# Kernel tuning notes

Hardware: AMD Instinct MI355X
Metric: run time of the kernel (lower is better)

## Reference

```python
import jax, jax.numpy as jnp
import numpy as np

N_NODES = 50000
N_EDGES = 800000
NUM_GRAPHS = 512


def gcn_conv(x, edge_index, W, b, num_nodes):
    # PyG GCNConv: h = D^{-1/2} (A + I) D^{-1/2} (x @ W) + b
    h = x @ W
    src, dst = edge_index[0], edge_index[1]
    loop = jnp.arange(num_nodes)
    src = jnp.concatenate([src, loop])
    dst = jnp.concatenate([dst, loop])
    deg = jax.ops.segment_sum(jnp.ones_like(dst, dtype=h.dtype), dst,
                              num_segments=num_nodes)
    dinv = jnp.where(deg > 0, jax.lax.rsqrt(deg), 0.0)
    norm = dinv[src] * dinv[dst]                      # [E+N]
    msg = h[src] * norm[:, None]                      # gather + scale
    out = jax.ops.segment_sum(msg, dst, num_segments=num_nodes)  # scatter-add
    return out + b


def global_mean_pool(x, batch, num_graphs):
    sums = jax.ops.segment_sum(x, batch, num_segments=num_graphs)
    cnts = jax.ops.segment_sum(jnp.ones((x.shape[0],), x.dtype), batch,
                               num_segments=num_graphs)
    return sums / jnp.maximum(cnts, 1.0)[:, None]


def setup_inputs() -> dict:
    key = jax.random.key(0)
    ks = jax.random.split(key, 8)
    x = jax.random.normal(ks[0], (N_NODES, 128), dtype=jnp.float32)
    edge_index = jax.random.randint(ks[1], (2, N_EDGES), 0, N_NODES, dtype=jnp.int64)
    batch = jnp.sort(jax.random.randint(ks[2], (N_NODES,), 0, NUM_GRAPHS, dtype=jnp.int64))
    W1 = jax.random.normal(ks[3], (128, 128), dtype=jnp.float32) * (1.0 / np.sqrt(128))
    b1 = jnp.zeros((128,), jnp.float32)
    W2 = jax.random.normal(ks[4], (128, 64), dtype=jnp.float32) * (1.0 / np.sqrt(128))
    b2 = jnp.zeros((64,), jnp.float32)
    Wl = jax.random.normal(ks[5], (64, 64), dtype=jnp.float32) * (1.0 / np.sqrt(64))
    bl = jnp.zeros((64,), jnp.float32)
    return {"x": x, "edge_index": edge_index, "batch": batch,
            "W1": W1, "b1": b1, "W2": W2, "b2": b2, "Wl": Wl, "bl": bl}


def reference(x, edge_index, batch, W1, b1, W2, b2, Wl, bl):
    num_nodes = x.shape[0]
    h = gcn_conv(x, edge_index, W1, b1, num_nodes)
    h = jax.nn.relu(h)
    h = gcn_conv(h, edge_index, W2, b2, num_nodes)
    g = global_mean_pool(h, batch, NUM_GRAPHS)
    # dropout p=0.5 is identity in eval mode
    return g @ Wl + bl
```

## Files before the change

kernel.cpp:

```cpp
#include <hip/hip_runtime.h>
#include <hip/hip_fp16.h>
#include <math.h>


#define FEAT1 128
#define FEAT2 64
#define BCAP 8192

using half8 = __attribute__((ext_vector_type(8))) _Float16;
using f32x4 = __attribute__((ext_vector_type(4))) float;

__global__ __launch_bounds__(256) void prep(const float* __restrict__ W1,
                                            const float* __restrict__ W2,
                                            _Float16* __restrict__ Wt1,
                                            _Float16* __restrict__ Wt2,
                                            int* __restrict__ bcur,
                                            float* __restrict__ pooled,
                                            int nb, int npool) {
    const int i = blockIdx.x * 256 + threadIdx.x;
    if (i < nb) bcur[i] = 0;
    const int j = i - nb;
    if (j >= 0 && j < npool) pooled[j] = 0.0f;
    if (i < 128 * 128) {
        int k = i & 127, c = i >> 7;
        Wt1[c * 128 + k] = (_Float16)W1[k * 128 + c];
    }
    if (i < 64 * 128) {
        int k = i & 127, c = i >> 7;
        Wt2[c * 128 + k] = (_Float16)W2[k * 64 + c];
    }
}


__global__ __launch_bounds__(256) void bin_scatter(const int* __restrict__ esrc,
                                                   const int* __restrict__ edst,
                                                   int ne, int nb,
                                                   int* __restrict__ bucket_cursor,
                                                   int* __restrict__ ebin) {
    __shared__ int lcnt[256];
    __shared__ int lcur[256];
    const int tid = threadIdx.x;
    const int e0 = blockIdx.x * 8192;
    int dcache[32];
    lcnt[tid] = 0;
    __syncthreads();
    #pragma unroll
    for (int k = 0; k < 32; k++) {
        int e = e0 + k * 256 + tid;
        dcache[k] = (e < ne) ? edst[e] : -1;
        if (dcache[k] >= 0) atomicAdd(&lcnt[dcache[k] >> 8], 1);
    }
    __syncthreads();
    if (tid < nb && lcnt[tid] > 0)
        lcur[tid] = atomicAdd(&bucket_cursor[tid], lcnt[tid]);
    __syncthreads();
    #pragma unroll
    for (int k = 0; k < 32; k++) {
        int d = dcache[k];
        if (d >= 0) {
            int e = e0 + k * 256 + tid;
            int b = d >> 8;
            int p = atomicAdd(&lcur[b], 1);
            if (p < BCAP)
                ebin[b * BCAP + p] = esrc[e] | ((d & 255) << 18);
        }
    }
}

__global__ __launch_bounds__(256) void bucket_csr(const int* __restrict__ ebin,
                                                  const int* __restrict__ bucket_cursor,
                                                  int n_nodes,
                                                  int* __restrict__ csr,
                                                  int2* __restrict__ nodeinfo,
                                                  float* __restrict__ dinv) {
    __shared__ int lcnt[256];
    __shared__ int lscan[256];
    __shared__ int lcur[256];
    const int b = blockIdx.x;
    const int tid = threadIdx.x;
    const int ebeg = b * BCAP;
    int cnt_b = bucket_cursor[b];
    if (cnt_b > BCAP) cnt_b = BCAP;
    const int eend = ebeg + cnt_b;
    lcnt[tid] = 0;
    __syncthreads();
    for (int e = ebeg + tid; e < eend; e += 256)
        atomicAdd(&lcnt[(ebin[e] >> 18) & 255], 1);
    __syncthreads();
    int v = lcnt[tid];
    lscan[tid] = v;
    __syncthreads();
    for (int off = 1; off < 256; off <<= 1) {
        int u = (tid >= off) ? lscan[tid - off] : 0;
        __syncthreads();
        lscan[tid] += u;
        __syncthreads();
    }
    const int start = ebeg + (lscan[tid] - v);
    const int node = (b << 8) + tid;
    if (node < n_nodes) {
        nodeinfo[node] = make_int2(start, v);
        dinv[node] = (float)(1.0 / sqrt((double)(v + 1)));
    }
    lcur[tid] = start;
    __syncthreads();
    for (int e = ebeg + tid; e < eend; e += 256) {
        int pk = ebin[e];
        int p = atomicAdd(&lcur[(pk >> 18) & 255], 1);
        csr[p] = pk & 0x3FFFF;
    }
}

template <int FOUT, bool A_F16>
__global__ __launch_bounds__(256) void gemm_direct(const void* __restrict__ Aptr,
                                                   const _Float16* __restrict__ Wt,
                                                   const float* __restrict__ dinv,
                                                   _Float16* __restrict__ out, int n) {
    const int wv = threadIdx.x >> 6;
    const int lane = threadIdx.x & 63;
    const int row0 = blockIdx.x * 128 + wv * 32;
    const int r16 = lane & 15;
    const int kb = (lane >> 4) * 8;

    half8 afrag[2][4];
    #pragma unroll
    for (int mi = 0; mi < 2; mi++) {
        const int grow = row0 + mi * 16 + r16;
        #pragma unroll
        for (int ks = 0; ks < 4; ks++) {
            if constexpr (A_F16) {
                half8 v = {};
                if (grow < n)
                    v = *(const half8*)((const _Float16*)Aptr + (size_t)grow * 128 + ks * 32 + kb);
                afrag[mi][ks] = v;
            } else {
                float4 v0 = {0.f, 0.f, 0.f, 0.f}, v1 = {0.f, 0.f, 0.f, 0.f};
                if (grow < n) {
                    const float* p = (const float*)Aptr + (size_t)grow * 128 + ks * 32 + kb;
                    v0 = *(const float4*)(p);
                    v1 = *(const float4*)(p + 4);
                }
                afrag[mi][ks] = half8{(_Float16)v0.x, (_Float16)v0.y, (_Float16)v0.z, (_Float16)v0.w,
                                      (_Float16)v1.x, (_Float16)v1.y, (_Float16)v1.z, (_Float16)v1.w};
            }
        }
    }

    #pragma unroll
    for (int ct = 0; ct < FOUT / 64; ct++) {
        const int col0 = ct * 64;
        f32x4 acc[2][4] = {};
        #pragma unroll
        for (int ks = 0; ks < 4; ks++) {
            #pragma unroll
            for (int nj = 0; nj < 4; nj++) {
                half8 b = *(const half8*)(Wt + (size_t)(col0 + nj * 16 + r16) * 128 + ks * 32 + kb);
                acc[0][nj] = __builtin_amdgcn_mfma_f32_16x16x32_f16(afrag[0][ks], b, acc[0][nj], 0, 0, 0);
                acc[1][nj] = __builtin_amdgcn_mfma_f32_16x16x32_f16(afrag[1][ks], b, acc[1][nj], 0, 0, 0);
            }
        }
        #pragma unroll
        for (int mi = 0; mi < 2; mi++) {
            const int gr0 = row0 + mi * 16 + (lane >> 4) * 4;
            #pragma unroll
            for (int r = 0; r < 4; r++) {
                const int grow = gr0 + r;
                if (grow < n) {
                    const float s = dinv[grow];
                    #pragma unroll
                    for (int nj = 0; nj < 4; nj++) {
                        out[(size_t)grow * FOUT + col0 + nj * 16 + r16] =
                            (_Float16)(acc[mi][nj][r] * s);
                    }
                }
            }
        }
    }
}

__global__ __launch_bounds__(256) void aggregate_l1(const __half* __restrict__ t,
                                                    const float* __restrict__ dinv,
                                                    const int2* __restrict__ nodeinfo,
                                                    const int* __restrict__ csr_src,
                                                    const float* __restrict__ bias,
                                                    __half* __restrict__ outp, int n) {
    constexpr int F = 128;
    const int wv = threadIdx.x >> 6;
    const int lane = threadIdx.x & 63;
    const int i = blockIdx.x * 4 + wv;
    if (i >= n) return;
    const float di = dinv[i];
    const int2 ni = nodeinfo[i];
    const int e0 = ni.x, e1 = ni.x + ni.y;

    float2 a0, a1 = {0.f, 0.f}, a2 = {0.f, 0.f}, a3 = {0.f, 0.f};
    a0 = __half22float2(((const __half2*)(t + (size_t)i * F))[lane]);
    int e = e0;
    for (; e + 8 <= e1; e += 8) {
        int s0 = csr_src[e + 0], s1 = csr_src[e + 1], s2 = csr_src[e + 2], s3 = csr_src[e + 3];
        int s4 = csr_src[e + 4], s5 = csr_src[e + 5], s6 = csr_src[e + 6], s7 = csr_src[e + 7];
        float2 v0 = __half22float2(((const __half2*)(t + (size_t)s0 * F))[lane]);
        float2 v1 = __half22float2(((const __half2*)(t + (size_t)s1 * F))[lane]);
        float2 v2 = __half22float2(((const __half2*)(t + (size_t)s2 * F))[lane]);
        float2 v3 = __half22float2(((const __half2*)(t + (size_t)s3 * F))[lane]);
        float2 v4 = __half22float2(((const __half2*)(t + (size_t)s4 * F))[lane]);
        float2 v5 = __half22float2(((const __half2*)(t + (size_t)s5 * F))[lane]);
        float2 v6 = __half22float2(((const __half2*)(t + (size_t)s6 * F))[lane]);
        float2 v7 = __half22float2(((const __half2*)(t + (size_t)s7 * F))[lane]);
        a0.x += v0.x + v4.x; a0.y += v0.y + v4.y;
        a1.x += v1.x + v5.x; a1.y += v1.y + v5.y;
        a2.x += v2.x + v6.x; a2.y += v2.y + v6.y;
        a3.x += v3.x + v7.x; a3.y += v3.y + v7.y;
    }
    for (; e + 4 <= e1; e += 4) {
        int s0 = csr_src[e + 0], s1 = csr_src[e + 1], s2 = csr_src[e + 2], s3 = csr_src[e + 3];
        float2 v0 = __half22float2(((const __half2*)(t + (size_t)s0 * F))[lane]);
        float2 v1 = __half22float2(((const __half2*)(t + (size_t)s1 * F))[lane]);
        float2 v2 = __half22float2(((const __half2*)(t + (size_t)s2 * F))[lane]);
        float2 v3 = __half22float2(((const __half2*)(t + (size_t)s3 * F))[lane]);
        a0.x += v0.x; a0.y += v0.y;
        a1.x += v1.x; a1.y += v1.y;
        a2.x += v2.x; a2.y += v2.y;
        a3.x += v3.x; a3.y += v3.y;
    }
    for (; e < e1; e++) {
        int s = csr_src[e];
        float2 v = __half22float2(((const __half2*)(t + (size_t)s * F))[lane]);
        a0.x += v.x; a0.y += v.y;
    }
    float2 b = ((const float2*)bias)[lane];
    float rx = (a0.x + a1.x + a2.x + a3.x) * di + b.x;
    float ry = (a0.y + a1.y + a2.y + a3.y) * di + b.y;
    rx = fmaxf(rx, 0.f); ry = fmaxf(ry, 0.f);
    ((__half2*)(outp + (size_t)i * F))[lane] = __floats2half2_rn(rx, ry);
}

__global__ __launch_bounds__(256) void aggregate_pool(const __half* __restrict__ t,
                                                      const float* __restrict__ dinv,
                                                      const int2* __restrict__ nodeinfo,
                                                      const int* __restrict__ csr_src,
                                                      const int* __restrict__ batch,
                                                      float* __restrict__ pooled_sums, int n) {
    constexpr int F = 64;
    const int wv = threadIdx.x >> 6;
    const int lane = threadIdx.x & 63;
    const int i = blockIdx.x * 4 + wv;
    if (i >= n) return;
    const float di = dinv[i];
    const int2 ni = nodeinfo[i];
    const int e0 = ni.x, e1 = ni.x + ni.y;

    float a0, a1 = 0.f, a2 = 0.f, a3 = 0.f;
    a0 = __half2float(t[(size_t)i * F + lane]);
    int e = e0;
    for (; e + 8 <= e1; e += 8) {
        int s0 = csr_src[e + 0], s1 = csr_src[e + 1], s2 = csr_src[e + 2], s3 = csr_src[e + 3];
        int s4 = csr_src[e + 4], s5 = csr_src[e + 5], s6 = csr_src[e + 6], s7 = csr_src[e + 7];
        float v0 = __half2float(t[(size_t)s0 * F + lane]);
        float v1 = __half2float(t[(size_t)s1 * F + lane]);
        float v2 = __half2float(t[(size_t)s2 * F + lane]);
        float v3 = __half2float(t[(size_t)s3 * F + lane]);
        float v4 = __half2float(t[(size_t)s4 * F + lane]);
        float v5 = __half2float(t[(size_t)s5 * F + lane]);
        float v6 = __half2float(t[(size_t)s6 * F + lane]);
        float v7 = __half2float(t[(size_t)s7 * F + lane]);
        a0 += v0 + v4; a1 += v1 + v5; a2 += v2 + v6; a3 += v3 + v7;
    }
    for (; e + 4 <= e1; e += 4) {
        int s0 = csr_src[e + 0], s1 = csr_src[e + 1], s2 = csr_src[e + 2], s3 = csr_src[e + 3];
        a0 += __half2float(t[(size_t)s0 * F + lane]);
        a1 += __half2float(t[(size_t)s1 * F + lane]);
        a2 += __half2float(t[(size_t)s2 * F + lane]);
        a3 += __half2float(t[(size_t)s3 * F + lane]);
    }
    for (; e < e1; e++) {
        a0 += __half2float(t[(size_t)csr_src[e] * F + lane]);
    }
    float r = (a0 + a1 + a2 + a3) * di;
    const int g = batch[i];
    atomicAdd(&pooled_sums[(size_t)g * F + lane], r);
}

__global__ __launch_bounds__(64) void classify(const float* __restrict__ pooled_sums,
                                               const int* __restrict__ batch, int n,
                                               const float* __restrict__ b2,
                                               const float* __restrict__ Wl,
                                               const float* __restrict__ bl,
                                               float* __restrict__ out) {
    __shared__ float pr[64];
    const int g = blockIdx.x;
    const int lane = threadIdx.x;
    int lo = 0, hi = n;
    while (lo < hi) { int mid = (lo + hi) >> 1; if (batch[mid] < g) lo = mid + 1; else hi = mid; }
    const int start = lo;
    hi = n;
    while (lo < hi) { int mid = (lo + hi) >> 1; if (batch[mid] < g + 1) lo = mid + 1; else hi = mid; }
    const float cnt = (float)(lo - start);
    float p = pooled_sums[(size_t)g * 64 + lane] / fmaxf(cnt, 1.0f) + b2[lane];
    pr[lane] = p;
    __syncthreads();
    float acc = bl[lane];
    #pragma unroll 8
    for (int k = 0; k < 64; k++) acc += pr[k] * Wl[k * 64 + lane];
    out[(size_t)g * 64 + lane] = acc;
}


extern "C" void kernel_launch(void* const* d_in, const int* in_sizes, int n_in,
                              void* d_out, int out_size, void* d_ws, size_t ws_size,
                              hipStream_t stream) {
    const float* x    = (const float*)d_in[0];
    const int*   eidx = (const int*)d_in[1];
    const int*   batch= (const int*)d_in[2];
    const float* W1   = (const float*)d_in[3];
    const float* b1   = (const float*)d_in[4];
    const float* W2   = (const float*)d_in[5];
    const float* b2   = (const float*)d_in[6];
    const float* Wl   = (const float*)d_in[7];
    const float* bl   = (const float*)d_in[8];
    float* out = (float*)d_out;

    const int n_nodes  = in_sizes[0] / FEAT1;
    const int n_edges  = in_sizes[1] / 2;
    const int n_graphs = out_size / FEAT2;
    const int* esrc = eidx;
    const int* edst = eidx + n_edges;
    const int nb = (n_nodes + 255) >> 8;
    const int npool = n_graphs * FEAT2;

    char* ws = (char*)d_ws;
    size_t off = 0;
    auto alloc = [&](size_t bytes) -> void* {
        void* p = ws + off;
        off += (bytes + 255) & ~(size_t)255;
        return p;
    };
    _Float16* t1     = (_Float16*)alloc((size_t)n_nodes * FEAT1 * 2);
    __half*   h1h    = (__half*)alloc((size_t)n_nodes * FEAT1 * 2);
    float*    dinv   = (float*)alloc((size_t)n_nodes * 4);
    int2*   nodeinfo = (int2*)alloc((size_t)n_nodes * 8);
    int*    bcur     = (int*)alloc((size_t)nb * 4);
    float*  pooled   = (float*)alloc((size_t)npool * 4);
    _Float16* Wt1    = (_Float16*)alloc(128 * 128 * 2);
    _Float16* Wt2    = (_Float16*)alloc(64 * 128 * 2);
    int*    ebin     = (int*)alloc((size_t)nb * BCAP * 4);
    int*    csr      = (int*)alloc((size_t)nb * BCAP * 4);

    const int nrb = (n_nodes + 127) / 128;

    prep<<<(nb + npool + 255) / 256, 256, 0, stream>>>(W1, W2, Wt1, Wt2, bcur, pooled, nb, npool);
    bin_scatter<<<(n_edges + 8191) / 8192, 256, 0, stream>>>(esrc, edst, n_edges, nb, bcur, ebin);
    bucket_csr<<<nb, 256, 0, stream>>>(ebin, bcur, n_nodes, csr, nodeinfo, dinv);

    gemm_direct<FEAT1, false><<<nrb, 256, 0, stream>>>(x, Wt1, dinv, t1, n_nodes);
    aggregate_l1<<<(n_nodes + 3) / 4, 256, 0, stream>>>(
        (const __half*)t1, dinv, nodeinfo, csr, b1, h1h, n_nodes);

    gemm_direct<FEAT2, true><<<nrb, 256, 0, stream>>>(h1h, Wt2, dinv, t1, n_nodes);
    aggregate_pool<<<(n_nodes + 3) / 4, 256, 0, stream>>>(
        (const __half*)t1, dinv, nodeinfo, csr, batch, pooled, n_nodes);

    classify<<<n_graphs, 64, 0, stream>>>(pooled, batch, n_nodes, b2, Wl, bl, out);
}
```

Before: 151.4 us.

## Fuse CSR build with layer-1 GEMM and layer-1 aggregation with layer-2 GEMM

The bucket CSR build and the layer-1 GEMM now run as one launch, with different block ranges doing independent work. The GEMM no longer needs the degree scaling, which moves into the gather as a per-source dinv multiply. The layer-1 aggregation now does the layer-2 GEMM per node through an LDS staging buffer and MFMA, so the intermediate h1 buffer is never written to or read from global memory. bin_scatter uses smaller per-block edge chunks. The costs are extra dinv gathers per edge and MFMA work wasted on replicated single-row tiles.

Result: slower. 197.5 us (+30.4%).

```diff
diff --git a/kernel.cpp b/kernel.cpp
--- a/kernel.cpp
+++ b/kernel.cpp
@@ -31,7 +31,6 @@
     }
 }
 
-
 __global__ __launch_bounds__(256) void bin_scatter(const int* __restrict__ esrc,
                                                    const int* __restrict__ edst,
                                                    int ne, int nb,
@@ -40,12 +39,12 @@
     __shared__ int lcnt[256];
     __shared__ int lcur[256];
     const int tid = threadIdx.x;
-    const int e0 = blockIdx.x * 8192;
-    int dcache[32];
+    const int e0 = blockIdx.x * 2048;
+    int dcache[8];
     lcnt[tid] = 0;
     __syncthreads();
     #pragma unroll
-    for (int k = 0; k < 32; k++) {
+    for (int k = 0; k < 8; k++) {
         int e = e0 + k * 256 + tid;
         dcache[k] = (e < ne) ? edst[e] : -1;
         if (dcache[k] >= 0) atomicAdd(&lcnt[dcache[k] >> 8], 1);
@@ -55,7 +54,7 @@
         lcur[tid] = atomicAdd(&bucket_cursor[tid], lcnt[tid]);
     __syncthreads();
     #pragma unroll
-    for (int k = 0; k < 32; k++) {
+    for (int k = 0; k < 8; k++) {
         int d = dcache[k];
         if (d >= 0) {
             int e = e0 + k * 256 + tid;
@@ -67,76 +66,68 @@
     }
 }
 
-__global__ __launch_bounds__(256) void bucket_csr(const int* __restrict__ ebin,
-                                                  const int* __restrict__ bucket_cursor,
-                                                  int n_nodes,
-                                                  int* __restrict__ csr,
-                                                  int2* __restrict__ nodeinfo,
-                                                  float* __restrict__ dinv) {
-    __shared__ int lcnt[256];
-    __shared__ int lscan[256];
-    __shared__ int lcur[256];
-    const int b = blockIdx.x;
-    const int tid = threadIdx.x;
-    const int ebeg = b * BCAP;
-    int cnt_b = bucket_cursor[b];
-    if (cnt_b > BCAP) cnt_b = BCAP;
-    const int eend = ebeg + cnt_b;
-    lcnt[tid] = 0;
-    __syncthreads();
-    for (int e = ebeg + tid; e < eend; e += 256)
-        atomicAdd(&lcnt[(ebin[e] >> 18) & 255], 1);
-    __syncthreads();
-    int v = lcnt[tid];
-    lscan[tid] = v;
-    __syncthreads();
-    for (int off = 1; off < 256; off <<= 1) {
-        int u = (tid >= off) ? lscan[tid - off] : 0;
+__global__ __launch_bounds__(256) void csr_gemm1(const int* __restrict__ ebin,
+                                                 const int* __restrict__ bucket_cursor,
+                                                 int n_nodes, int nb,
+                                                 int* __restrict__ csr,
+                                                 int2* __restrict__ nodeinfo,
+                                                 float* __restrict__ dinv,
+                                                 const float* __restrict__ A,
+                                                 const _Float16* __restrict__ Wt1,
+                                                 _Float16* __restrict__ t1raw) {
+    if ((int)blockIdx.x < nb) {
+        __shared__ int lcnt[256];
+        __shared__ int lscan[256];
+        __shared__ int lcur[256];
+        const int b = blockIdx.x;
+        const int tid = threadIdx.x;
+        const int ebeg = b * BCAP;
+        int cnt_b = bucket_cursor[b];
+        if (cnt_b > BCAP) cnt_b = BCAP;
+        const int eend = ebeg + cnt_b;
+        lcnt[tid] = 0;
         __syncthreads();
-        lscan[tid] += u;
+        for (int e = ebeg + tid; e < eend; e += 256)
+            atomicAdd(&lcnt[(ebin[e] >> 18) & 255], 1);
         __syncthreads();
-    }
-    const int start = ebeg + (lscan[tid] - v);
-    const int node = (b << 8) + tid;
-    if (node < n_nodes) {
-        nodeinfo[node] = make_int2(start, v);
-        dinv[node] = (float)(1.0 / sqrt((double)(v + 1)));
-    }
-    lcur[tid] = start;
-    __syncthreads();
-    for (int e = ebeg + tid; e < eend; e += 256) {
-        int pk = ebin[e];
-        int p = atomicAdd(&lcur[(pk >> 18) & 255], 1);
-        csr[p] = pk & 0x3FFFF;
-    }
-}
-
-template <int FOUT, bool A_F16>
-__global__ __launch_bounds__(256) void gemm_direct(const void* __restrict__ Aptr,
-                                                   const _Float16* __restrict__ Wt,
-                                                   const float* __restrict__ dinv,
-                                                   _Float16* __restrict__ out, int n) {
-    const int wv = threadIdx.x >> 6;
-    const int lane = threadIdx.x & 63;
-    const int row0 = blockIdx.x * 128 + wv * 32;
-    const int r16 = lane & 15;
-    const int kb = (lane >> 4) * 8;
-
-    half8 afrag[2][4];
-    #pragma unroll
-    for (int mi = 0; mi < 2; mi++) {
-        const int grow = row0 + mi * 16 + r16;
+        int v = lcnt[tid];
+        lscan[tid] = v;
+        __syncthreads();
+        for (int off = 1; off < 256; off <<= 1) {
+            int u = (tid >= off) ? lscan[tid - off] : 0;
+            __syncthreads();
+            lscan[tid] += u;
+            __syncthreads();
+        }
+        const int start = ebeg + (lscan[tid] - v);
+        const int node = (b << 8) + tid;
+        if (node < n_nodes) {
+            nodeinfo[node] = make_int2(start, v);
+            dinv[node] = (float)(1.0 / sqrt((double)(v + 1)));
+        }
+        lcur[tid] = start;
+        __syncthreads();
+        for (int e = ebeg + tid; e < eend; e += 256) {
+            int pk = ebin[e];
+            int p = atomicAdd(&lcur[(pk >> 18) & 255], 1);
+            csr[p] = pk & 0x3FFFF;
+        }
+    } else {
+        const int wv = threadIdx.x >> 6;
+        const int lane = threadIdx.x & 63;
+        const int row0 = (blockIdx.x - nb) * 128 + wv * 32;
+        const int r16 = lane & 15;
+        const int kb = (lane >> 4) * 8;
+
+        half8 afrag[2][4];
         #pragma unroll
-        for (int ks = 0; ks < 4; ks++) {
-            if constexpr (A_F16) {
-                half8 v = {};
-                if (grow < n)
-                    v = *(const half8*)((const _Float16*)Aptr + (size_t)grow * 128 + ks * 32 + kb);
-                afrag[mi][ks] = v;
-            } else {
+        for (int mi = 0; mi < 2; mi++) {
+            const int grow = row0 + mi * 16 + r16;
+            #pragma unroll
+            for (int ks = 0; ks < 4; ks++) {
                 float4 v0 = {0.f, 0.f, 0.f, 0.f}, v1 = {0.f, 0.f, 0.f, 0.f};
-                if (grow < n) {
-                    const float* p = (const float*)Aptr + (size_t)grow * 128 + ks * 32 + kb;
+                if (grow < n_nodes) {
+                    const float* p = A + (size_t)grow * 128 + ks * 32 + kb;
                     v0 = *(const float4*)(p);
                     v1 = *(const float4*)(p + 4);
                 }
@@ -144,33 +135,30 @@
                                       (_Float16)v1.x, (_Float16)v1.y, (_Float16)v1.z, (_Float16)v1.w};
             }
         }
-    }
-
-    #pragma unroll
-    for (int ct = 0; ct < FOUT / 64; ct++) {
-        const int col0 = ct * 64;
-        f32x4 acc[2][4] = {};
         #pragma unroll
-        for (int ks = 0; ks < 4; ks++) {
+        for (int ct = 0; ct < 2; ct++) {
+            const int col0 = ct * 64;
+            f32x4 acc[2][4] = {};
             #pragma unroll
-            for (int nj = 0; nj < 4; nj++) {
-                half8 b = *(const half8*)(Wt + (size_t)(col0 + nj * 16 + r16) * 128 + ks * 32 + kb);
-                acc[0][nj] = __builtin_amdgcn_mfma_f32_16x16x32_f16(afrag[0][ks], b, acc[0][nj], 0, 0, 0);
-                acc[1][nj] = __builtin_amdgcn_mfma_f32_16x16x32_f16(afrag[1][ks], b, acc[1][nj], 0, 0, 0);
+            for (int ks = 0; ks < 4; ks++) {
+                #pragma unroll
+                for (int nj = 0; nj < 4; nj++) {
+                    half8 b = *(const half8*)(Wt1 + (size_t)(col0 + nj * 16 + r16) * 128 + ks * 32 + kb);
+                    acc[0][nj] = __builtin_amdgcn_mfma_f32_16x16x32_f16(afrag[0][ks], b, acc[0][nj], 0, 0, 0);
+                    acc[1][nj] = __builtin_amdgcn_mfma_f32_16x16x32_f16(afrag[1][ks], b, acc[1][nj], 0, 0, 0);
+                }
             }
-        }
-        #pragma unroll
-        for (int mi = 0; mi < 2; mi++) {
-            const int gr0 = row0 + mi * 16 + (lane >> 4) * 4;
             #pragma unroll
-            for (int r = 0; r < 4; r++) {
-                const int grow = gr0 + r;
-                if (grow < n) {
-                    const float s = dinv[grow];
-                    #pragma unroll
-                    for (int nj = 0; nj < 4; nj++) {
-                        out[(size_t)grow * FOUT + col0 + nj * 16 + r16] =
-                            (_Float16)(acc[mi][nj][r] * s);
+            for (int mi = 0; mi < 2; mi++) {
+                const int gr0 = row0 + mi * 16 + (lane >> 4) * 4;
+                #pragma unroll
+                for (int r = 0; r < 4; r++) {
+                    const int grow = gr0 + r;
+                    if (grow < n_nodes) {
+                        #pragma unroll
+                        for (int nj = 0; nj < 4; nj++)
+                            t1raw[(size_t)grow * 128 + col0 + nj * 16 + r16] =
+                                (_Float16)acc[mi][nj][r];
                     }
                 }
             }
@@ -178,13 +166,15 @@
     }
 }
 
-__global__ __launch_bounds__(256) void aggregate_l1(const __half* __restrict__ t,
-                                                    const float* __restrict__ dinv,
-                                                    const int2* __restrict__ nodeinfo,
-                                                    const int* __restrict__ csr_src,
-                                                    const float* __restrict__ bias,
-                                                    __half* __restrict__ outp, int n) {
+__global__ __launch_bounds__(256) void agg1_gemm2(const __half* __restrict__ t,
+                                                  const float* __restrict__ dinv,
+                                                  const int2* __restrict__ nodeinfo,
+                                                  const int* __restrict__ csr_src,
+                                                  const float* __restrict__ bias,
+                                                  const _Float16* __restrict__ Wt2,
+                                                  _Float16* __restrict__ t2, int n) {
     constexpr int F = 128;
+    __shared__ _Float16 hlds[4][128];
     const int wv = threadIdx.x >> 6;
     const int lane = threadIdx.x & 63;
     const int i = blockIdx.x * 4 + wv;
@@ -194,11 +184,16 @@
     const int e0 = ni.x, e1 = ni.x + ni.y;
 
     float2 a0, a1 = {0.f, 0.f}, a2 = {0.f, 0.f}, a3 = {0.f, 0.f};
-    a0 = __half22float2(((const __half2*)(t + (size_t)i * F))[lane]);
+    {
+        float2 v = __half22float2(((const __half2*)(t + (size_t)i * F))[lane]);
+        a0.x = v.x * di; a0.y = v.y * di;
+    }
     int e = e0;
     for (; e + 8 <= e1; e += 8) {
         int s0 = csr_src[e + 0], s1 = csr_src[e + 1], s2 = csr_src[e + 2], s3 = csr_src[e + 3];
         int s4 = csr_src[e + 4], s5 = csr_src[e + 5], s6 = csr_src[e + 6], s7 = csr_src[e + 7];
+        float d0 = dinv[s0], d1 = dinv[s1], d2 = dinv[s2], d3 = dinv[s3];
+        float d4 = dinv[s4], d5 = dinv[s5], d6 = dinv[s6], d7 = dinv[s7];
         float2 v0 = __half22float2(((const __half2*)(t + (size_t)s0 * F))[lane]);
         float2 v1 = __half22float2(((const __half2*)(t + (size_t)s1 * F))[lane]);
         float2 v2 = __half22float2(((const __half2*)(t + (size_t)s2 * F))[lane]);
@@ -207,32 +202,52 @@
         float2 v5 = __half22float2(((const __half2*)(t + (size_t)s5 * F))[lane]);
         float2 v6 = __half22float2(((const __half2*)(t + (size_t)s6 * F))[lane]);
         float2 v7 = __half22float2(((const __half2*)(t + (size_t)s7 * F))[lane]);
-        a0.x += v0.x + v4.x; a0.y += v0.y + v4.y;
-        a1.x += v1.x + v5.x; a1.y += v1.y + v5.y;
-        a2.x += v2.x + v6.x; a2.y += v2.y + v6.y;
-        a3.x += v3.x + v7.x; a3.y += v3.y + v7.y;
+        a0.x += v0.x * d0 + v4.x * d4; a0.y += v0.y * d0 + v4.y * d4;
+        a1.x += v1.x * d1 + v5.x * d5; a1.y += v1.y * d1 + v5.y * d5;
+        a2.x += v2.x * d2 + v6.x * d6; a2.y += v2.y * d2 + v6.y * d6;
+        a3.x += v3.x * d3 + v7.x * d7; a3.y += v3.y * d3 + v7.y * d7;
     }
     for (; e + 4 <= e1; e += 4) {
         int s0 = csr_src[e + 0], s1 = csr_src[e + 1], s2 = csr_src[e + 2], s3 = csr_src[e + 3];
+        float d0 = dinv[s0], d1 = dinv[s1], d2 = dinv[s2], d3 = dinv[s3];
         float2 v0 = __half22float2(((const __half2*)(t + (size_t)s0 * F))[lane]);
         float2 v1 = __half22float2(((const __half2*)(t + (size_t)s1 * F))[lane]);
         float2 v2 = __half22float2(((const __half2*)(t + (size_t)s2 * F))[lane]);
         float2 v3 = __half22float2(((const __half2*)(t + (size_t)s3 * F))[lane]);
-        a0.x += v0.x; a0.y += v0.y;
-        a1.x += v1.x; a1.y += v1.y;
-        a2.x += v2.x; a2.y += v2.y;
-        a3.x += v3.x; a3.y += v3.y;
+        a0.x += v0.x * d0; a0.y += v0.y * d0;
+        a1.x += v1.x * d1; a1.y += v1.y * d1;
+        a2.x += v2.x * d2; a2.y += v2.y * d2;
+        a3.x += v3.x * d3; a3.y += v3.y * d3;
     }
     for (; e < e1; e++) {
         int s = csr_src[e];
+        float d = dinv[s];
         float2 v = __half22float2(((const __half2*)(t + (size_t)s * F))[lane]);
-        a0.x += v.x; a0.y += v.y;
+        a0.x += v.x * d; a0.y += v.y * d;
     }
     float2 b = ((const float2*)bias)[lane];
     float rx = (a0.x + a1.x + a2.x + a3.x) * di + b.x;
     float ry = (a0.y + a1.y + a2.y + a3.y) * di + b.y;
     rx = fmaxf(rx, 0.f); ry = fmaxf(ry, 0.f);
-    ((__half2*)(outp + (size_t)i * F))[lane] = __floats2half2_rn(rx, ry);
+
+    ((__half2*)hlds[wv])[lane] = __floats2half2_rn(rx, ry);
+    const int r16 = lane & 15;
+    const int kb = (lane >> 4) * 8;
+    f32x4 acc[4] = {};
+    #pragma unroll
+    for (int ks = 0; ks < 4; ks++) {
+        half8 af = *(const half8*)(&hlds[wv][ks * 32 + kb]);
+        #pragma unroll
+        for (int nj = 0; nj < 4; nj++) {
+            half8 bf = *(const half8*)(Wt2 + (size_t)(nj * 16 + r16) * 128 + ks * 32 + kb);
+            acc[nj] = __builtin_amdgcn_mfma_f32_16x16x32_f16(af, bf, acc[nj], 0, 0, 0);
+        }
+    }
+    if (lane < 16) {
+        #pragma unroll
+        for (int nj = 0; nj < 4; nj++)
+            t2[(size_t)i * 64 + nj * 16 + lane] = (_Float16)(acc[nj][0] * di);
+    }
 }
 
 __global__ __launch_bounds__(256) void aggregate_pool(const __half* __restrict__ t,
@@ -335,8 +350,8 @@
         off += (bytes + 255) & ~(size_t)255;
         return p;
     };
-    _Float16* t1     = (_Float16*)alloc((size_t)n_nodes * FEAT1 * 2);
-    __half*   h1h    = (__half*)alloc((size_t)n_nodes * FEAT1 * 2);
+    _Float16* t1raw  = (_Float16*)alloc((size_t)n_nodes * FEAT1 * 2);
+    _Float16* t2     = (_Float16*)alloc((size_t)n_nodes * FEAT2 * 2);
     float*    dinv   = (float*)alloc((size_t)n_nodes * 4);
     int2*   nodeinfo = (int2*)alloc((size_t)n_nodes * 8);
     int*    bcur     = (int*)alloc((size_t)nb * 4);
@@ -349,16 +364,12 @@
     const int nrb = (n_nodes + 127) / 128;
 
     prep<<<(nb + npool + 255) / 256, 256, 0, stream>>>(W1, W2, Wt1, Wt2, bcur, pooled, nb, npool);
-    bin_scatter<<<(n_edges + 8191) / 8192, 256, 0, stream>>>(esrc, edst, n_edges, nb, bcur, ebin);
-    bucket_csr<<<nb, 256, 0, stream>>>(ebin, bcur, n_nodes, csr, nodeinfo, dinv);
-
-    gemm_direct<FEAT1, false><<<nrb, 256, 0, stream>>>(x, Wt1, dinv, t1, n_nodes);
-    aggregate_l1<<<(n_nodes + 3) / 4, 256, 0, stream>>>(
-        (const __half*)t1, dinv, nodeinfo, csr, b1, h1h, n_nodes);
-
-    gemm_direct<FEAT2, true><<<nrb, 256, 0, stream>>>(h1h, Wt2, dinv, t1, n_nodes);
+    bin_scatter<<<(n_edges + 2047) / 2048, 256, 0, stream>>>(esrc, edst, n_edges, nb, bcur, ebin);
+    csr_gemm1<<<nb + nrb, 256, 0, stream>>>(ebin, bcur, n_nodes, nb, csr, nodeinfo, dinv,
+                                            x, Wt1, t1raw);
+    agg1_gemm2<<<(n_nodes + 3) / 4, 256, 0, stream>>>(
+        (const __half*)t1raw, dinv, nodeinfo, csr, b1, Wt2, t2, n_nodes);
     aggregate_pool<<<(n_nodes + 3) / 4, 256, 0, stream>>>(
-        (const __half*)t1, dinv, nodeinfo, csr, batch, pooled, n_nodes);
-
+        (const __half*)t2, dinv, nodeinfo, csr, batch, pooled, n_nodes);
     classify<<<n_graphs, 64, 0, stream>>>(pooled, batch, n_nodes, b2, Wl, bl, out);
 }
```

## Fuse layer-2 GEMM into layer-1 aggregation kernel via per-node MFMA

Applied to the files above, without the earlier changes.

Each wave's ReLU'd layer-1 row is staged in LDS and multiplied straight away by Wt2 with MFMA, writing the scaled 64-wide layer-2 features. This removes the separate second GEMM launch and the write and re-read of the 128-wide fp16 intermediate. In exchange, each wave runs a 16-row MFMA with only one useful row and re-reads the full Wt2 from cache, which adds redundant compute and cache traffic per node. The GEMM kernel is simplified to its layer-1-only form.

After: 210.0 us. +38.7%, slower.

```diff
diff --git a/kernel.cpp b/kernel.cpp
--- a/kernel.cpp
+++ b/kernel.cpp
@@ -30,7 +30,6 @@
         Wt2[c * 128 + k] = (_Float16)W2[k * 64 + c];
     }
 }
-
 
 __global__ __launch_bounds__(256) void bin_scatter(const int* __restrict__ esrc,
                                                    const int* __restrict__ edst,
@@ -111,8 +110,7 @@
     }
 }
 
-template <int FOUT, bool A_F16>
-__global__ __launch_bounds__(256) void gemm_direct(const void* __restrict__ Aptr,
+__global__ __launch_bounds__(256) void gemm_direct(const float* __restrict__ A,
                                                    const _Float16* __restrict__ Wt,
                                                    const float* __restrict__ dinv,
                                                    _Float16* __restrict__ out, int n) {
@@ -128,26 +126,19 @@
         const int grow = row0 + mi * 16 + r16;
         #pragma unroll
         for (int ks = 0; ks < 4; ks++) {
-            if constexpr (A_F16) {
-                half8 v = {};
-                if (grow < n)
-                    v = *(const half8*)((const _Float16*)Aptr + (size_t)grow * 128 + ks * 32 + kb);
-                afrag[mi][ks] = v;
-            } else {
-                float4 v0 = {0.f, 0.f, 0.f, 0.f}, v1 = {0.f, 0.f, 0.f, 0.f};
-                if (grow < n) {
-                    const float* p = (const float*)Aptr + (size_t)grow * 128 + ks * 32 + kb;
-                    v0 = *(const float4*)(p);
-                    v1 = *(const float4*)(p + 4);
-                }
-                afrag[mi][ks] = half8{(_Float16)v0.x, (_Float16)v0.y, (_Float16)v0.z, (_Float16)v0.w,
-                                      (_Float16)v1.x, (_Float16)v1.y, (_Float16)v1.z, (_Float16)v1.w};
+            float4 v0 = {0.f, 0.f, 0.f, 0.f}, v1 = {0.f, 0.f, 0.f, 0.f};
+            if (grow < n) {
+                const float* p = A + (size_t)grow * 128 + ks * 32 + kb;
+                v0 = *(const float4*)(p);
+                v1 = *(const float4*)(p + 4);
             }
-        }
-    }
-
-    #pragma unroll
-    for (int ct = 0; ct < FOUT / 64; ct++) {
+            afrag[mi][ks] = half8{(_Float16)v0.x, (_Float16)v0.y, (_Float16)v0.z, (_Float16)v0.w,
+                                  (_Float16)v1.x, (_Float16)v1.y, (_Float16)v1.z, (_Float16)v1.w};
+        }
+    }
+
+    #pragma unroll
+    for (int ct = 0; ct < 2; ct++) {
         const int col0 = ct * 64;
         f32x4 acc[2][4] = {};
         #pragma unroll
@@ -168,23 +159,24 @@
                 if (grow < n) {
                     const float s = dinv[grow];
                     #pragma unroll
-                    for (int nj = 0; nj < 4; nj++) {
-                        out[(size_t)grow * FOUT + col0 + nj * 16 + r16] =
+                    for (int nj = 0; nj < 4; nj++)
+                        out[(size_t)grow * 128 + col0 + nj * 16 + r16] =
                             (_Float16)(acc[mi][nj][r] * s);
-                    }
                 }
             }
         }
     }
 }
 
-__global__ __launch_bounds__(256) void aggregate_l1(const __half* __restrict__ t,
-                                                    const float* __restrict__ dinv,
-                                                    const int2* __restrict__ nodeinfo,
-                                                    const int* __restrict__ csr_src,
-                                                    const float* __restrict__ bias,
-                                                    __half* __restrict__ outp, int n) {
+__global__ __launch_bounds__(256) void agg1_gemm2(const __half* __restrict__ t,
+                                                  const float* __restrict__ dinv,
+                                                  const int2* __restrict__ nodeinfo,
+                                                  const int* __restrict__ csr_src,
+                                                  const float* __restrict__ bias,
+                                                  const _Float16* __restrict__ Wt2,
+                                                  _Float16* __restrict__ t2, int n) {
     constexpr int F = 128;
+    __shared__ _Float16 hlds[4][128];
     const int wv = threadIdx.x >> 6;
     const int lane = threadIdx.x & 63;
     const int i = blockIdx.x * 4 + wv;
@@ -232,7 +224,25 @@
     float rx = (a0.x + a1.x + a2.x + a3.x) * di + b.x;
     float ry = (a0.y + a1.y + a2.y + a3.y) * di + b.y;
     rx = fmaxf(rx, 0.f); ry = fmaxf(ry, 0.f);
-    ((__half2*)(outp + (size_t)i * F))[lane] = __floats2half2_rn(rx, ry);
+
+    ((__half2*)hlds[wv])[lane] = __floats2half2_rn(rx, ry);
+    const int r16 = lane & 15;
+    const int kb = (lane >> 4) * 8;
+    f32x4 acc[4] = {};
+    #pragma unroll
+    for (int ks = 0; ks < 4; ks++) {
+        half8 af = *(const half8*)(&hlds[wv][ks * 32 + kb]);
+        #pragma unroll
+        for (int nj = 0; nj < 4; nj++) {
+            half8 bf = *(const half8*)(Wt2 + (size_t)(nj * 16 + r16) * 128 + ks * 32 + kb);
+            acc[nj] = __builtin_amdgcn_mfma_f32_16x16x32_f16(af, bf, acc[nj], 0, 0, 0);
+        }
+    }
+    if (lane < 16) {
+        #pragma unroll
+        for (int nj = 0; nj < 4; nj++)
+            t2[(size_t)i * 64 + nj * 16 + lane] = (_Float16)(acc[nj][0] * di);
+    }
 }
 
 __global__ __launch_bounds__(256) void aggregate_pool(const __half* __restrict__ t,
@@ -336,7 +346,7 @@
         return p;
     };
     _Float16* t1     = (_Float16*)alloc((size_t)n_nodes * FEAT1 * 2);
-    __half*   h1h    = (__half*)alloc((size_t)n_nodes * FEAT1 * 2);
+    _Float16* t2     = (_Float16*)alloc((size_t)n_nodes * FEAT2 * 2);
     float*    dinv   = (float*)alloc((size_t)n_nodes * 4);
     int2*   nodeinfo = (int2*)alloc((size_t)n_nodes * 8);
     int*    bcur     = (int*)alloc((size_t)nb * 4);
@@ -351,14 +361,10 @@
     prep<<<(nb + npool + 255) / 256, 256, 0, stream>>>(W1, W2, Wt1, Wt2, bcur, pooled, nb, npool);
     bin_scatter<<<(n_edges + 8191) / 8192, 256, 0, stream>>>(esrc, edst, n_edges, nb, bcur, ebin);
     bucket_csr<<<nb, 256, 0, stream>>>(ebin, bcur, n_nodes, csr, nodeinfo, dinv);
-
-    gemm_direct<FEAT1, false><<<nrb, 256, 0, stream>>>(x, Wt1, dinv, t1, n_nodes);
-    aggregate_l1<<<(n_nodes + 3) / 4, 256, 0, stream>>>(
-        (const __half*)t1, dinv, nodeinfo, csr, b1, h1h, n_nodes);
-
-    gemm_direct<FEAT2, true><<<nrb, 256, 0, stream>>>(h1h, Wt2, dinv, t1, n_nodes);
+    gemm_direct<<<nrb, 256, 0, stream>>>(x, Wt1, dinv, t1, n_nodes);
+    agg1_gemm2<<<(n_nodes + 3) / 4, 256, 0, stream>>>(
+        (const __half*)t1, dinv, nodeinfo, csr, b1, Wt2, t2, n_nodes);
     aggregate_pool<<<(n_nodes + 3) / 4, 256, 0, stream>>>(
-        (const __half*)t1, dinv, nodeinfo, csr, batch, pooled, n_nodes);
-
+        (const __half*)t2, dinv, nodeinfo, csr, batch, pooled, n_nodes);
     classify<<<n_graphs, 64, 0, stream>>>(pooled, batch, n_nodes, b2, Wl, bl, out);
 }
```
